# Kernel optimization log

Hardware: AMD Instinct MI355X
Metric: run time of the kernel (lower is better)

## Reference

```python
import jax, jax.numpy as jnp
import numpy as np

N_NODES = 100000
N_EDGES = 1600000
IN_FEAT = 128
EMBED = 64
N_LAYERS = 3
N_CENTROID = 100
N_CLASS = 10
EPS = 1e-12


def setup_inputs() -> dict:
    key = jax.random.key(0)
    ks = jax.random.split(key, 8)
    x = jax.random.normal(ks[0], (N_NODES, IN_FEAT), dtype=jnp.float32)
    edge_index = jax.random.randint(ks[1], (2, N_EDGES), 0, N_NODES, dtype=jnp.int64)
    W_embed = jax.random.normal(ks[2], (EMBED, IN_FEAT), dtype=jnp.float32) / np.sqrt(IN_FEAT)
    W_gcn = jax.random.normal(ks[3], (N_LAYERS, EMBED, EMBED), dtype=jnp.float32) / np.sqrt(EMBED)
    b_gcn = jnp.zeros((N_LAYERS, EMBED), dtype=jnp.float32)
    centroids = jax.random.normal(ks[4], (N_CENTROID, EMBED), dtype=jnp.float32)
    W_out = jax.random.normal(ks[5], (N_CLASS, N_CENTROID), dtype=jnp.float32) / np.sqrt(N_CENTROID)
    b_out = jnp.zeros((N_CLASS,), dtype=jnp.float32)
    return {"x": x, "edge_index": edge_index, "W_embed": W_embed, "W_gcn": W_gcn,
            "b_gcn": b_gcn, "centroids": centroids, "W_out": W_out, "b_out": b_out}


def _gcn_norm(edge_index, n, dtype):
    # add self loops, compute symmetric D^{-1/2}(A+I)D^{-1/2} edge weights
    loops = jnp.arange(n, dtype=edge_index.dtype)
    src = jnp.concatenate([edge_index[0], loops])
    dst = jnp.concatenate([edge_index[1], loops])
    deg = jax.ops.segment_sum(jnp.ones_like(dst, dtype=dtype), dst, num_segments=n)
    dinv = jax.lax.rsqrt(jnp.maximum(deg, 1.0))
    norm = dinv[src] * dinv[dst]  # [E+N]
    return src, dst, norm


def reference(x, edge_index, W_embed, W_gcn, b_gcn, centroids, W_out, b_out):
    n = x.shape[0]
    src, dst, norm = _gcn_norm(edge_index, n, x.dtype)
    # Euclidean manifold: log/exp are identity
    h = x @ W_embed.T  # [N, D]
    for l in range(W_gcn.shape[0]):
        hw = h @ W_gcn[l].T                                   # [N, D]
        msg = hw[src] * norm[:, None]                         # gather  [E+N, D]
        h = jax.ops.segment_sum(msg, dst, num_segments=n)     # scatter [N, D]
        h = jax.nn.relu(h + b_gcn[l])
    # centroid distances: ||h_i - c_k|| via expanded quadratic (avoids [N,K,D])
    h2 = jnp.sum(h * h, axis=-1, keepdims=True)               # [N, 1]
    c2 = jnp.sum(centroids * centroids, axis=-1)[None, :]     # [1, K]
    d2 = jnp.maximum(h2 + c2 - 2.0 * (h @ centroids.T), 0.0)  # [N, K]
    dist = jnp.sqrt(d2 + EPS)
    pooled = dist.mean(axis=0)                                # [K] graph pooling
    return pooled @ W_out.T + b_out                           # [num_class]
```

## Files before the change

kernel.cpp:

```cpp
#include <hip/hip_runtime.h>
#include <hip/hip_bf16.h>

typedef unsigned int uint32;
typedef float floatx2 __attribute__((ext_vector_type(2)));
typedef __attribute__((ext_vector_type(8))) short bf16x8;
typedef __attribute__((ext_vector_type(4))) float f32x4;

#define CHUNK 16384


__global__ __launch_bounds__(256) void k_bhist(const int* __restrict__ dst,
                                               int* __restrict__ bcnt,
                                               int E, int NBUCK, int NCH) {
    __shared__ int h[512];
    int c = blockIdx.x, tid = threadIdx.x;
    for (int i = tid; i < NBUCK; i += 256) h[i] = 0;
    __syncthreads();
    int base = c * CHUNK;
#pragma unroll
    for (int k = 0; k < CHUNK / 256; ++k) {
        int e = base + k * 256 + tid;
        if (e < E) atomicAdd(&h[dst[e] >> 8], 1);
    }
    __syncthreads();
    for (int i = tid; i < NBUCK; i += 256) bcnt[(size_t)i * NCH + c] = h[i];
}

__global__ __launch_bounds__(128) void k_bscan1(const int* __restrict__ bcnt,
                                                int* __restrict__ bofs,
                                                int* __restrict__ btot, int NCH) {
    __shared__ int tmp[128];
    int b = blockIdx.x, t = threadIdx.x;
    int v = (t < NCH) ? bcnt[(size_t)b * NCH + t] : 0;
    tmp[t] = v;
    __syncthreads();
    for (int off = 1; off < 128; off <<= 1) {
        int u = (t >= off) ? tmp[t - off] : 0;
        __syncthreads();
        tmp[t] += u;
        __syncthreads();
    }
    if (t < NCH) bofs[(size_t)b * NCH + t] = tmp[t] - v;
    if (t == 127) btot[b] = tmp[127];
}

__global__ __launch_bounds__(512) void k_bscan2(const int* __restrict__ btot,
                                                int* __restrict__ bbase, int nb) {
    __shared__ int tmp[512];
    int t = threadIdx.x;
    int v = (t < nb) ? btot[t] : 0;
    tmp[t] = v;
    __syncthreads();
    for (int off = 1; off < 512; off <<= 1) {
        int u = (t >= off) ? tmp[t - off] : 0;
        __syncthreads();
        tmp[t] += u;
        __syncthreads();
    }
    if (t < nb) bbase[t] = tmp[t] - v;
    if (t == nb - 1) bbase[nb] = tmp[t];
}

__global__ __launch_bounds__(256) void k_bscatter(const int* __restrict__ ei,
                                                  const int* __restrict__ bbase,
                                                  const int* __restrict__ bofs,
                                                  uint32* __restrict__ ebuf,
                                                  int E, int NBUCK, int NCH) {
    __shared__ int cur[512];
    int c = blockIdx.x, tid = threadIdx.x;
    for (int i = tid; i < NBUCK; i += 256)
        cur[i] = bbase[i] + bofs[(size_t)i * NCH + c];
    __syncthreads();
    int base = c * CHUNK;
#pragma unroll
    for (int k = 0; k < CHUNK / 256; ++k) {
        int e = base + k * 256 + tid;
        if (e < E) {
            int s = ei[e];
            int d = ei[E + e];
            int p = atomicAdd(&cur[d >> 8], 1);
            ebuf[p] = (uint32)s | ((uint32)(d & 255) << 20);
        }
    }
}

__global__ __launch_bounds__(256) void k_bsort(const uint32* __restrict__ ebuf,
                                               const int* __restrict__ bbase,
                                               int* __restrict__ ssrc,
                                               int2* __restrict__ rc,
                                               float* __restrict__ dinv, int N) {
    __shared__ int h[256];
    __shared__ int sc[256];
    __shared__ int cur[256];
    int b = blockIdx.x, tid = threadIdx.x;
    int beg = bbase[b], end = bbase[b + 1];
    h[tid] = 0;
    __syncthreads();
    for (int j = beg + tid; j < end; j += 256)
        atomicAdd(&h[(ebuf[j] >> 20) & 255], 1);
    __syncthreads();
    int v = h[tid];
    sc[tid] = v;
    __syncthreads();
    for (int off = 1; off < 256; off <<= 1) {
        int u = (tid >= off) ? sc[tid - off] : 0;
        __syncthreads();
        sc[tid] += u;
        __syncthreads();
    }
    int rowbase = beg + sc[tid] - v;
    cur[tid] = rowbase;
    int d = b * 256 + tid;
    if (d < N) {
        rc[d] = make_int2(rowbase, v);
        dinv[d] = rsqrtf((float)(v + 1));
    }
    __syncthreads();
    for (int j = beg + tid; j < end; j += 256) {
        uint32 w = ebuf[j];
        int p = atomicAdd(&cur[(w >> 20) & 255], 1);
        ssrc[p] = (int)(w & 0xFFFFFu);
    }
}


__device__ __forceinline__ short f2bf(float f) {
    __hip_bfloat16 b = __float2bfloat16(f);
    return __builtin_bit_cast(short, b);
}

__device__ __forceinline__ float bf2f(short s) {
    uint32 u = ((uint32)(unsigned short)s) << 16;
    return __builtin_bit_cast(float, u);
}

__device__ __forceinline__ bf16x8 pack_bf16x8(float4 v0, float4 v1) {
    bf16x8 r;
    r[0] = f2bf(v0.x); r[1] = f2bf(v0.y); r[2] = f2bf(v0.z); r[3] = f2bf(v0.w);
    r[4] = f2bf(v1.x); r[5] = f2bf(v1.y); r[6] = f2bf(v1.z); r[7] = f2bf(v1.w);
    return r;
}


__global__ __launch_bounds__(256) void k_embed(const float* __restrict__ x,
                                               const float* __restrict__ We,
                                               short* __restrict__ h, int N) {
    int lane = threadIdx.x & 63;
    int w = threadIdx.x >> 6;
    int l15 = lane & 15;
    int lg = lane >> 4;

    bf16x8 B[4][4];
#pragma unroll
    for (int ct = 0; ct < 4; ++ct) {
        const float* wr = We + (size_t)(ct * 16 + l15) * 128 + lg * 8;
#pragma unroll
        for (int ks = 0; ks < 4; ++ks) {
            float4 v0 = *(const float4*)(wr + ks * 32);
            float4 v1 = *(const float4*)(wr + ks * 32 + 4);
            B[ct][ks] = pack_bf16x8(v0, v1);
        }
    }

    int rowbase = blockIdx.x * 256 + w * 64;

    f32x4 acc[4][4];
#pragma unroll
    for (int rt = 0; rt < 4; ++rt)
#pragma unroll
        for (int ct = 0; ct < 4; ++ct)
            acc[rt][ct] = (f32x4){0.f, 0.f, 0.f, 0.f};

#pragma unroll
    for (int ks = 0; ks < 4; ++ks) {
#pragma unroll
        for (int rt = 0; rt < 4; ++rt) {
            int row = rowbase + rt * 16 + l15;
            row = (row < N) ? row : (N - 1);
            const float* xr = x + (size_t)row * 128 + ks * 32 + lg * 8;
            float4 v0 = *(const float4*)xr;
            float4 v1 = *(const float4*)(xr + 4);
            bf16x8 a = pack_bf16x8(v0, v1);
#pragma unroll
            for (int ct = 0; ct < 4; ++ct)
                acc[rt][ct] = __builtin_amdgcn_mfma_f32_16x16x32_bf16(
                    a, B[ct][ks], acc[rt][ct], 0, 0, 0);
        }
    }

#pragma unroll
    for (int rt = 0; rt < 4; ++rt) {
        int row0 = rowbase + rt * 16 + lg * 4;
#pragma unroll
        for (int r = 0; r < 4; ++r) {
            int row = row0 + r;
            if (row < N) {
#pragma unroll
                for (int ct = 0; ct < 4; ++ct)
                    h[(size_t)row * 64 + ct * 16 + l15] = f2bf(acc[rt][ct][r]);
            }
        }
    }
}


__global__ __launch_bounds__(256) void k_gcn(const short* __restrict__ hin,
                                             const float* __restrict__ Wg,
                                             const float* __restrict__ dinv,
                                             uint32* __restrict__ tab0,
                                             uint32* __restrict__ tab1, int N) {
    int lane = threadIdx.x & 63;
    int w = threadIdx.x >> 6;
    int l15 = lane & 15, lg = lane >> 4;

    bf16x8 A[4][2];
#pragma unroll
    for (int rt = 0; rt < 4; ++rt) {
        const float* wr = Wg + (size_t)(rt * 16 + l15) * 64 + lg * 8;
#pragma unroll
        for (int ks = 0; ks < 2; ++ks) {
            float4 v0 = *(const float4*)(wr + ks * 32);
            float4 v1 = *(const float4*)(wr + ks * 32 + 4);
            A[rt][ks] = pack_bf16x8(v0, v1);
        }
    }

    int nodebase = blockIdx.x * 256 + w * 64;

#pragma unroll
    for (int nt = 0; nt < 4; ++nt) {
        int node = nodebase + nt * 16 + l15;
        int nodec = (node < N) ? node : (N - 1);
        const short* hr = hin + ((size_t)nodec << 6) + lg * 8;

        bf16x8 Bf0 = *(const bf16x8*)(hr);
        bf16x8 Bf1 = *(const bf16x8*)(hr + 32);

        f32x4 acc[4];
#pragma unroll
        for (int rt = 0; rt < 4; ++rt) acc[rt] = (f32x4){0.f, 0.f, 0.f, 0.f};
#pragma unroll
        for (int rt = 0; rt < 4; ++rt)
            acc[rt] = __builtin_amdgcn_mfma_f32_16x16x32_bf16(A[rt][0], Bf0, acc[rt], 0, 0, 0);
#pragma unroll
        for (int rt = 0; rt < 4; ++rt)
            acc[rt] = __builtin_amdgcn_mfma_f32_16x16x32_bf16(A[rt][1], Bf1, acc[rt], 0, 0, 0);

        float s = dinv[nodec];
        if (node < N) {
#pragma unroll
            for (int rt = 0; rt < 4; ++rt) {
                int u = 0;
                u = __builtin_amdgcn_cvt_pk_fp8_f32(acc[rt][0] * s, acc[rt][1] * s, u, false);
                u = __builtin_amdgcn_cvt_pk_fp8_f32(acc[rt][2] * s, acc[rt][3] * s, u, true);
                uint32* tp = (rt < 2) ? tab0 : tab1;
                tp[(size_t)node * 8 + (rt & 1) * 4 + lg] = u;
            }
        }
    }
}


__global__ __launch_bounds__(256) void k_agg(const int2* __restrict__ rc,
                                             const int* __restrict__ ssrc,
                                             const float* __restrict__ dinv,
                                             const uint2* __restrict__ tabh,
                                             short* __restrict__ outh,
                                             const float* __restrict__ bias,
                                             int N, int E) {
    int lane = threadIdx.x & 63;
    int wid = threadIdx.x >> 6;
    int q = lane & 3;
    int g = lane >> 2;
    int dbase = (blockIdx.x * 4 + wid) * 16;
    if (dbase >= N) return;

    int2 r = rc[min(dbase + (lane & 15), N - 1)];
    int beg = __shfl(r.x, g);
    int deg = __shfl(r.y, g);
    int dg = dbase + g;
    if (dg >= N) deg = 0;

    floatx2 a01 = {0.f, 0.f}, a23 = {0.f, 0.f}, a45 = {0.f, 0.f}, a67 = {0.f, 0.f};
    auto accum = [&](uint2 v) {
        a01 += __builtin_amdgcn_cvt_pk_f32_fp8((int)v.x, false);
        a23 += __builtin_amdgcn_cvt_pk_f32_fp8((int)v.x, true);
        a45 += __builtin_amdgcn_cvt_pk_f32_fp8((int)v.y, false);
        a67 += __builtin_amdgcn_cvt_pk_f32_fp8((int)v.y, true);
    };

    accum(tabh[(size_t)((dg < N) ? dg : N) * 4 + q]);

    int m = deg;
    m = max(m, __shfl_xor(m, 4));
    m = max(m, __shfl_xor(m, 8));
    m = max(m, __shfl_xor(m, 16));
    m = max(m, __shfl_xor(m, 32));
    int maxd = __builtin_amdgcn_readfirstlane(m);

    int base4 = lane & 60;
    for (int j = 0; j < maxd; j += 8) {
        int i0 = beg + j + q;
        int i1 = i0 + 4;
        int ev0 = ssrc[i0 < E ? i0 : 0];
        int ev1 = ssrc[i1 < E ? i1 : 0];
        int t0 = __shfl(ev0, base4 | 0);
        int t1 = __shfl(ev0, base4 | 1);
        int t2 = __shfl(ev0, base4 | 2);
        int t3 = __shfl(ev0, base4 | 3);
        int t4 = __shfl(ev1, base4 | 0);
        int t5 = __shfl(ev1, base4 | 1);
        int t6 = __shfl(ev1, base4 | 2);
        int t7 = __shfl(ev1, base4 | 3);
        t0 = (j + 0 < deg) ? t0 : N;
        t1 = (j + 1 < deg) ? t1 : N;
        t2 = (j + 2 < deg) ? t2 : N;
        t3 = (j + 3 < deg) ? t3 : N;
        t4 = (j + 4 < deg) ? t4 : N;
        t5 = (j + 5 < deg) ? t5 : N;
        t6 = (j + 6 < deg) ? t6 : N;
        t7 = (j + 7 < deg) ? t7 : N;
        uint2 v0 = tabh[(size_t)t0 * 4 + q];
        uint2 v1 = tabh[(size_t)t1 * 4 + q];
        uint2 v2 = tabh[(size_t)t2 * 4 + q];
        uint2 v3 = tabh[(size_t)t3 * 4 + q];
        uint2 v4 = tabh[(size_t)t4 * 4 + q];
        uint2 v5 = tabh[(size_t)t5 * 4 + q];
        uint2 v6 = tabh[(size_t)t6 * 4 + q];
        uint2 v7 = tabh[(size_t)t7 * 4 + q];
        accum(v0); accum(v1); accum(v2); accum(v3);
        accum(v4); accum(v5); accum(v6); accum(v7);
    }

    if (dg < N) {
        float dd = dinv[dg];
        float4 b0 = *(const float4*)(bias + q * 8);
        float4 b1 = *(const float4*)(bias + q * 8 + 4);
        bf16x8 o;
        o[0] = f2bf(fmaxf(fmaf(dd, a01.x, b0.x), 0.f));
        o[1] = f2bf(fmaxf(fmaf(dd, a01.y, b0.y), 0.f));
        o[2] = f2bf(fmaxf(fmaf(dd, a23.x, b0.z), 0.f));
        o[3] = f2bf(fmaxf(fmaf(dd, a23.y, b0.w), 0.f));
        o[4] = f2bf(fmaxf(fmaf(dd, a45.x, b1.x), 0.f));
        o[5] = f2bf(fmaxf(fmaf(dd, a45.y, b1.y), 0.f));
        o[6] = f2bf(fmaxf(fmaf(dd, a67.x, b1.z), 0.f));
        o[7] = f2bf(fmaxf(fmaf(dd, a67.y, b1.w), 0.f));
        __builtin_nontemporal_store(o, (bf16x8*)(outh + (size_t)dg * 64 + q * 8));
    }
}


__global__ void k_c2(const float* __restrict__ C, float* __restrict__ c2) {
    int k = threadIdx.x;
    if (k < 100) {
        float s = 0.f;
        for (int d = 0; d < 64; ++d) { float v = C[k * 64 + d]; s = fmaf(v, v, s); }
        c2[k] = s;
    }
}


__global__ __launch_bounds__(256) void k_cent(const short* __restrict__ hin,
                                              const float* __restrict__ C,
                                              const float* __restrict__ c2g,
                                              float* __restrict__ partials, int N) {
    __shared__ float pool4[4][112];
    __shared__ float h2_s[128];
    int tid = threadIdx.x;
    int lane = tid & 63, w = tid >> 6;
    int l15 = lane & 15, lg = lane >> 4;

    bf16x8 B[7][2];
#pragma unroll
    for (int ct = 0; ct < 7; ++ct) {
        int col = ct * 16 + l15;
#pragma unroll
        for (int ks = 0; ks < 2; ++ks) {
            float4 v0 = make_float4(0.f, 0.f, 0.f, 0.f);
            float4 v1 = make_float4(0.f, 0.f, 0.f, 0.f);
            if (col < 100) {
                const float* cr = C + (size_t)col * 64 + ks * 32 + lg * 8;
                v0 = *(const float4*)cr;
                v1 = *(const float4*)(cr + 4);
            }
            B[ct][ks] = pack_bf16x8(v0, v1);
        }
    }

    int rowbase = blockIdx.x * 128 + w * 32;

    f32x4 acc[2][7];
#pragma unroll
    for (int rt = 0; rt < 2; ++rt)
#pragma unroll
        for (int ct = 0; ct < 7; ++ct)
            acc[rt][ct] = (f32x4){0.f, 0.f, 0.f, 0.f};

#pragma unroll
    for (int rt = 0; rt < 2; ++rt) {
        int row = rowbase + rt * 16 + l15;
        int rowc = (row < N) ? row : (N - 1);
        const short* hr = hin + ((size_t)rowc << 6) + lg * 8;
        bf16x8 a0 = *(const bf16x8*)(hr);
        bf16x8 a1 = *(const bf16x8*)(hr + 32);

        float h2p = 0.f;
#pragma unroll
        for (int j = 0; j < 8; ++j) {
            float v0 = bf2f(a0[j]);
            float v1 = bf2f(a1[j]);
            h2p = fmaf(v0, v0, h2p);
            h2p = fmaf(v1, v1, h2p);
        }
        h2p += __shfl_xor(h2p, 16);
        h2p += __shfl_xor(h2p, 32);
        if (lg == 0) h2_s[w * 32 + rt * 16 + l15] = h2p;

#pragma unroll
        for (int ct = 0; ct < 7; ++ct)
            acc[rt][ct] = __builtin_amdgcn_mfma_f32_16x16x32_bf16(
                a0, B[ct][0], acc[rt][ct], 0, 0, 0);
#pragma unroll
        for (int ct = 0; ct < 7; ++ct)
            acc[rt][ct] = __builtin_amdgcn_mfma_f32_16x16x32_bf16(
                a1, B[ct][1], acc[rt][ct], 0, 0, 0);
    }

    float S[7] = {0.f, 0.f, 0.f, 0.f, 0.f, 0.f, 0.f};
#pragma unroll
    for (int rt = 0; rt < 2; ++rt) {
#pragma unroll
        for (int r = 0; r < 4; ++r) {
            int row = rowbase + rt * 16 + lg * 4 + r;
            float h2v = h2_s[w * 32 + rt * 16 + lg * 4 + r];
            bool rv = row < N;
#pragma unroll
            for (int ct = 0; ct < 7; ++ct) {
                int col = ct * 16 + l15;
                float c2v = (col < 100) ? c2g[col] : 0.f;
                float G = acc[rt][ct][r];
                float d2 = fmaxf(h2v + c2v - 2.f * G, 0.f);
                float xx = d2 + 1e-12f;
                float dist = xx * __frsqrt_rn(xx);
                S[ct] += (rv && col < 100) ? dist : 0.f;
            }
        }
    }
#pragma unroll
    for (int ct = 0; ct < 7; ++ct) {
        float s = S[ct];
        s += __shfl_xor(s, 16);
        s += __shfl_xor(s, 32);
        if (lg == 0) pool4[w][ct * 16 + l15] = s;
    }
    __syncthreads();
    if (tid < 112) {
        float s = pool4[0][tid] + pool4[1][tid] + pool4[2][tid] + pool4[3][tid];
        partials[(size_t)blockIdx.x * 128 + tid] = s;
    }
}


__global__ __launch_bounds__(1024) void k_out(const float* __restrict__ partials, int nb,
                                              const float* __restrict__ Wout,
                                              const float* __restrict__ bout,
                                              float* __restrict__ out, float invN) {
    __shared__ float ps[8][112];
    int t = threadIdx.x & 127, g = threadIdx.x >> 7;
    if (t < 112) {
        float s0 = 0.f, s1 = 0.f, s2 = 0.f, s3 = 0.f;
        float s4 = 0.f, s5 = 0.f, s6 = 0.f, s7 = 0.f;
        int b = g;
        for (; b + 56 < nb; b += 64) {
            s0 += partials[(size_t)(b     ) * 128 + t];
            s1 += partials[(size_t)(b +  8) * 128 + t];
            s2 += partials[(size_t)(b + 16) * 128 + t];
            s3 += partials[(size_t)(b + 24) * 128 + t];
            s4 += partials[(size_t)(b + 32) * 128 + t];
            s5 += partials[(size_t)(b + 40) * 128 + t];
            s6 += partials[(size_t)(b + 48) * 128 + t];
            s7 += partials[(size_t)(b + 56) * 128 + t];
        }
        for (; b < nb; b += 8) s0 += partials[(size_t)b * 128 + t];
        ps[g][t] = ((s0 + s1) + (s2 + s3)) + ((s4 + s5) + (s6 + s7));
    }
    __syncthreads();
    if (threadIdx.x < 10) {
        int tt = threadIdx.x;
        float s = 0.f;
        for (int k = 0; k < 100; ++k) {
            float p = ps[0][k] + ps[1][k] + ps[2][k] + ps[3][k]
                    + ps[4][k] + ps[5][k] + ps[6][k] + ps[7][k];
            s = fmaf(p, Wout[tt * 100 + k], s);
        }
        out[tt] = s * invN + bout[tt];
    }
}


extern "C" void kernel_launch(void* const* d_in, const int* in_sizes, int n_in,
                              void* d_out, int out_size, void* d_ws, size_t ws_size,
                              hipStream_t stream) {
    const float* x    = (const float*)d_in[0];
    const int*   ei   = (const int*)d_in[1];
    const float* We   = (const float*)d_in[2];
    const float* Wg   = (const float*)d_in[3];
    const float* bg   = (const float*)d_in[4];
    const float* C    = (const float*)d_in[5];
    const float* Wout = (const float*)d_in[6];
    const float* bout = (const float*)d_in[7];
    float*       out  = (float*)d_out;

    const int N = in_sizes[0] / 128;
    const int E = in_sizes[1] / 2;
    const int NBUCK = (N + 255) >> 8;
    const int NCH = (E + CHUNK - 1) / CHUNK;
    const int NBC = (N + 127) / 128;
    const int NBA = (N + 63) / 64;

    char* ws = (char*)d_ws;
    size_t off = 0;
    auto alloc = [&](size_t bytes) { void* p = ws + off; off += (bytes + 511) & ~(size_t)511; return p; };
    float*  dinv   = (float*)alloc((size_t)N * 4);
    int2*   rc     = (int2*) alloc((size_t)N * 8);
    int*    bcnt   = (int*)  alloc((size_t)NBUCK * NCH * 4);
    int*    bofs   = (int*)  alloc((size_t)NBUCK * NCH * 4);
    int*    btot   = (int*)  alloc((size_t)NBUCK * 4);
    int*    bbase  = (int*)  alloc((size_t)(NBUCK + 1) * 4);
    uint32* ebuf   = (uint32*)alloc((size_t)E * 4);
    int*    ssrc   = (int*)  alloc((size_t)(E + 64) * 4);
    short*  hA     = (short*)alloc((size_t)N * 64 * 2);
    uint32* tab0   = (uint32*)alloc((size_t)(N + 1) * 32);
    uint32* tab1   = (uint32*)alloc((size_t)(N + 1) * 32);
    float*  c2     = (float*)alloc(512);
    float*  partials = (float*)alloc((size_t)NBC * 128 * 4);

    hipMemsetAsync(tab0 + (size_t)N * 8, 0, 32, stream);
    hipMemsetAsync(tab1 + (size_t)N * 8, 0, 32, stream);

    k_bhist<<<NCH, 256, 0, stream>>>(ei + E, bcnt, E, NBUCK, NCH);
    k_bscan1<<<NBUCK, 128, 0, stream>>>(bcnt, bofs, btot, NCH);
    k_bscan2<<<1, 512, 0, stream>>>(btot, bbase, NBUCK);
    k_bscatter<<<NCH, 256, 0, stream>>>(ei, bbase, bofs, ebuf, E, NBUCK, NCH);
    k_bsort<<<NBUCK, 256, 0, stream>>>(ebuf, bbase, ssrc, rc, dinv, N);
    k_c2<<<1, 128, 0, stream>>>(C, c2);

    k_embed<<<(N + 255) / 256, 256, 0, stream>>>(x, We, hA, N);

    for (int l = 0; l < 3; ++l) {
        k_gcn<<<(N + 255) / 256, 256, 0, stream>>>(hA, Wg + (size_t)l * 64 * 64,
                                                   dinv, tab0, tab1, N);
        k_agg<<<NBA, 256, 0, stream>>>(rc, ssrc, dinv, (const uint2*)tab0,
                                       hA, bg + (size_t)l * 64, N, E);
        k_agg<<<NBA, 256, 0, stream>>>(rc, ssrc, dinv, (const uint2*)tab1,
                                       hA + 32, bg + (size_t)l * 64 + 32, N, E);
    }

    k_cent<<<NBC, 256, 0, stream>>>(hA, C, c2, partials, N);

    k_out<<<1, 1024, 0, stream>>>(partials, NBC, Wout, bout, out, 1.0f / (float)N);
}
```

Measured before the change: 348.9 us.

## Unroll aggregation gather to 16 edges and fold small launches into existing kernels

The neighbor-aggregation loop now processes 16 edges per iteration instead of 8, putting more independent gathers in flight per wave. The separate centroid-norm kernel is removed and each k_cent block computes the norms in registers with shuffles. The two sentinel-row memsets are folded into the scan kernel. Together these cut launch and memset overhead and aim to raise memory-level parallelism in the gather, at the cost of higher register pressure and more wasted predicated loads for low-degree nodes.

```diff
diff --git a/kernel.cpp b/kernel.cpp
--- a/kernel.cpp
+++ b/kernel.cpp
@@ -45,9 +45,12 @@
 }
 
 __global__ __launch_bounds__(512) void k_bscan2(const int* __restrict__ btot,
-                                                int* __restrict__ bbase, int nb) {
+                                                int* __restrict__ bbase, int nb,
+                                                uint32* __restrict__ sent0,
+                                                uint32* __restrict__ sent1) {
     __shared__ int tmp[512];
     int t = threadIdx.x;
+    if (t < 8) { sent0[t] = 0; sent1[t] = 0; }
     int v = (t < nb) ? btot[t] : 0;
     tmp[t] = v;
     __syncthreads();
@@ -299,27 +302,47 @@
     int maxd = __builtin_amdgcn_readfirstlane(m);
 
     int base4 = lane & 60;
-    for (int j = 0; j < maxd; j += 8) {
+    for (int j = 0; j < maxd; j += 16) {
         int i0 = beg + j + q;
         int i1 = i0 + 4;
+        int i2 = i0 + 8;
+        int i3 = i0 + 12;
         int ev0 = ssrc[i0 < E ? i0 : 0];
         int ev1 = ssrc[i1 < E ? i1 : 0];
-        int t0 = __shfl(ev0, base4 | 0);
-        int t1 = __shfl(ev0, base4 | 1);
-        int t2 = __shfl(ev0, base4 | 2);
-        int t3 = __shfl(ev0, base4 | 3);
-        int t4 = __shfl(ev1, base4 | 0);
-        int t5 = __shfl(ev1, base4 | 1);
-        int t6 = __shfl(ev1, base4 | 2);
-        int t7 = __shfl(ev1, base4 | 3);
-        t0 = (j + 0 < deg) ? t0 : N;
-        t1 = (j + 1 < deg) ? t1 : N;
-        t2 = (j + 2 < deg) ? t2 : N;
-        t3 = (j + 3 < deg) ? t3 : N;
-        t4 = (j + 4 < deg) ? t4 : N;
-        t5 = (j + 5 < deg) ? t5 : N;
-        t6 = (j + 6 < deg) ? t6 : N;
-        t7 = (j + 7 < deg) ? t7 : N;
+        int ev2 = ssrc[i2 < E ? i2 : 0];
+        int ev3 = ssrc[i3 < E ? i3 : 0];
+        int t0  = __shfl(ev0, base4 | 0);
+        int t1  = __shfl(ev0, base4 | 1);
+        int t2  = __shfl(ev0, base4 | 2);
+        int t3  = __shfl(ev0, base4 | 3);
+        int t4  = __shfl(ev1, base4 | 0);
+        int t5  = __shfl(ev1, base4 | 1);
+        int t6  = __shfl(ev1, base4 | 2);
+        int t7  = __shfl(ev1, base4 | 3);
+        int t8  = __shfl(ev2, base4 | 0);
+        int t9  = __shfl(ev2, base4 | 1);
+        int ta  = __shfl(ev2, base4 | 2);
+        int tb  = __shfl(ev2, base4 | 3);
+        int tc  = __shfl(ev3, base4 | 0);
+        int td  = __shfl(ev3, base4 | 1);
+        int te  = __shfl(ev3, base4 | 2);
+        int tf  = __shfl(ev3, base4 | 3);
+        t0 = (j +  0 < deg) ? t0 : N;
+        t1 = (j +  1 < deg) ? t1 : N;
+        t2 = (j +  2 < deg) ? t2 : N;
+        t3 = (j +  3 < deg) ? t3 : N;
+        t4 = (j +  4 < deg) ? t4 : N;
+        t5 = (j +  5 < deg) ? t5 : N;
+        t6 = (j +  6 < deg) ? t6 : N;
+        t7 = (j +  7 < deg) ? t7 : N;
+        t8 = (j +  8 < deg) ? t8 : N;
+        t9 = (j +  9 < deg) ? t9 : N;
+        ta = (j + 10 < deg) ? ta : N;
+        tb = (j + 11 < deg) ? tb : N;
+        tc = (j + 12 < deg) ? tc : N;
+        td = (j + 13 < deg) ? td : N;
+        te = (j + 14 < deg) ? te : N;
+        tf = (j + 15 < deg) ? tf : N;
         uint2 v0 = tabh[(size_t)t0 * 4 + q];
         uint2 v1 = tabh[(size_t)t1 * 4 + q];
         uint2 v2 = tabh[(size_t)t2 * 4 + q];
@@ -328,8 +351,18 @@
         uint2 v5 = tabh[(size_t)t5 * 4 + q];
         uint2 v6 = tabh[(size_t)t6 * 4 + q];
         uint2 v7 = tabh[(size_t)t7 * 4 + q];
+        uint2 v8 = tabh[(size_t)t8 * 4 + q];
+        uint2 v9 = tabh[(size_t)t9 * 4 + q];
+        uint2 va = tabh[(size_t)ta * 4 + q];
+        uint2 vb = tabh[(size_t)tb * 4 + q];
+        uint2 vc = tabh[(size_t)tc * 4 + q];
+        uint2 vd = tabh[(size_t)td * 4 + q];
+        uint2 ve = tabh[(size_t)te * 4 + q];
+        uint2 vf = tabh[(size_t)tf * 4 + q];
         accum(v0); accum(v1); accum(v2); accum(v3);
         accum(v4); accum(v5); accum(v6); accum(v7);
+        accum(v8); accum(v9); accum(va); accum(vb);
+        accum(vc); accum(vd); accum(ve); accum(vf);
     }
 
     if (dg < N) {
@@ -350,19 +383,8 @@
 }
 
 
-__global__ void k_c2(const float* __restrict__ C, float* __restrict__ c2) {
-    int k = threadIdx.x;
-    if (k < 100) {
-        float s = 0.f;
-        for (int d = 0; d < 64; ++d) { float v = C[k * 64 + d]; s = fmaf(v, v, s); }
-        c2[k] = s;
-    }
-}
-
-
 __global__ __launch_bounds__(256) void k_cent(const short* __restrict__ hin,
                                               const float* __restrict__ C,
-                                              const float* __restrict__ c2g,
                                               float* __restrict__ partials, int N) {
     __shared__ float pool4[4][112];
     __shared__ float h2_s[128];
@@ -371,9 +393,11 @@
     int l15 = lane & 15, lg = lane >> 4;
 
     bf16x8 B[7][2];
+    float c2r[7];
 #pragma unroll
     for (int ct = 0; ct < 7; ++ct) {
         int col = ct * 16 + l15;
+        float c2p = 0.f;
 #pragma unroll
         for (int ks = 0; ks < 2; ++ks) {
             float4 v0 = make_float4(0.f, 0.f, 0.f, 0.f);
@@ -384,7 +408,14 @@
                 v1 = *(const float4*)(cr + 4);
             }
             B[ct][ks] = pack_bf16x8(v0, v1);
-        }
+            c2p = fmaf(v0.x, v0.x, c2p); c2p = fmaf(v0.y, v0.y, c2p);
+            c2p = fmaf(v0.z, v0.z, c2p); c2p = fmaf(v0.w, v0.w, c2p);
+            c2p = fmaf(v1.x, v1.x, c2p); c2p = fmaf(v1.y, v1.y, c2p);
+            c2p = fmaf(v1.z, v1.z, c2p); c2p = fmaf(v1.w, v1.w, c2p);
+        }
+        c2p += __shfl_xor(c2p, 16);
+        c2p += __shfl_xor(c2p, 32);
+        c2r[ct] = c2p;
     }
 
     int rowbase = blockIdx.x * 128 + w * 32;
@@ -437,9 +468,8 @@
 #pragma unroll
             for (int ct = 0; ct < 7; ++ct) {
                 int col = ct * 16 + l15;
-                float c2v = (col < 100) ? c2g[col] : 0.f;
                 float G = acc[rt][ct][r];
-                float d2 = fmaxf(h2v + c2v - 2.f * G, 0.f);
+                float d2 = fmaxf(h2v + c2r[ct] - 2.f * G, 0.f);
                 float xx = d2 + 1e-12f;
                 float dist = xx * __frsqrt_rn(xx);
                 S[ct] += (rv && col < 100) ? dist : 0.f;
@@ -532,18 +562,14 @@
     short*  hA     = (short*)alloc((size_t)N * 64 * 2);
     uint32* tab0   = (uint32*)alloc((size_t)(N + 1) * 32);
     uint32* tab1   = (uint32*)alloc((size_t)(N + 1) * 32);
-    float*  c2     = (float*)alloc(512);
     float*  partials = (float*)alloc((size_t)NBC * 128 * 4);
-
-    hipMemsetAsync(tab0 + (size_t)N * 8, 0, 32, stream);
-    hipMemsetAsync(tab1 + (size_t)N * 8, 0, 32, stream);
 
     k_bhist<<<NCH, 256, 0, stream>>>(ei + E, bcnt, E, NBUCK, NCH);
     k_bscan1<<<NBUCK, 128, 0, stream>>>(bcnt, bofs, btot, NCH);
-    k_bscan2<<<1, 512, 0, stream>>>(btot, bbase, NBUCK);
+    k_bscan2<<<1, 512, 0, stream>>>(btot, bbase, NBUCK,
+                                    tab0 + (size_t)N * 8, tab1 + (size_t)N * 8);
     k_bscatter<<<NCH, 256, 0, stream>>>(ei, bbase, bofs, ebuf, E, NBUCK, NCH);
     k_bsort<<<NBUCK, 256, 0, stream>>>(ebuf, bbase, ssrc, rc, dinv, N);
-    k_c2<<<1, 128, 0, stream>>>(C, c2);
 
     k_embed<<<(N + 255) / 256, 256, 0, stream>>>(x, We, hA, N);
 
@@ -556,7 +582,7 @@
                                        hA + 32, bg + (size_t)l * 64 + 32, N, E);
     }
 
-    k_cent<<<NBC, 256, 0, stream>>>(hA, C, c2, partials, N);
+    k_cent<<<NBC, 256, 0, stream>>>(hA, C, partials, N);
 
     k_out<<<1, 1024, 0, stream>>>(partials, NBC, Wout, bout, out, 1.0f / (float)N);
 }
```

Measured after the change: 339.0 us (median of 2 runs). 1.03x faster.
